# Kernel optimization log

Hardware: AMD Instinct MI355X
Metric: run time of the kernel (lower is better)

## Reference

```python
import jax, jax.numpy as jnp
import numpy as np
from jax import lax

KERNEL_SIZE = 3
SMOOTH_NR = 0.0
SMOOTH_DR = 1e-5


def _box_sum(x, k):
    # 3D box-filter sum with zero padding (matches F.conv3d padding=(k-1)//2),
    # x: [B, C, H, W, D]. 'SAME' padding with odd k and stride 1 == symmetric pad (k-1)//2.
    return lax.reduce_window(x, jnp.array(0.0, x.dtype), lax.add,
                             window_dimensions=(1, 1, k, k, k),
                             window_strides=(1, 1, 1, 1, 1),
                             padding='SAME')


def setup_inputs() -> dict:
    key = jax.random.key(0)
    k1, k2 = jax.random.split(key)
    shape = (2, 1, 192, 192, 192)
    pred = jax.random.uniform(k1, shape, dtype=jnp.float32)
    target = jax.random.uniform(k2, shape, dtype=jnp.float32)
    return {"pred": pred, "target": target}


def reference(pred, target):
    k = KERNEL_SIZE
    kvol = float(k ** 3)
    # Local means of I, J, I^2, J^2, I*J (box filter divided by kernel volume,
    # mirroring the torch code's avg_filt grouped conv over the 5C-channel interm).
    mI = _box_sum(pred, k) / kvol
    mJ = _box_sum(target, k) / kvol
    mII = _box_sum(pred * pred, k) / kvol
    mJJ = _box_sum(target * target, k) / kvol
    mIJ = _box_sum(pred * target, k) / kvol
    # Fused NCC reduction (cc3d_fwd_interm_v1): convert means back to
    # windowed sums-based cross/variance terms using kernel_vol.
    cross = kvol * (mIJ - mI * mJ)
    p_var = kvol * (mII - mI * mI)
    t_var = kvol * (mJJ - mJ * mJ)
    ncc = (cross * cross + SMOOTH_NR) / (t_var * p_var + SMOOTH_DR)
    # reduction='mean', loss is negated squared local ZNCC
    return -jnp.mean(ncc)
```

## Files before the change

kernel.cpp:

```cpp
#include <hip/hip_runtime.h>

#define DIMB 2
#define DIMS 192
#define DPT 4
#define TX 16
#define TY 16
#define HCHUNK 6
#define ROWF 72
#define ARR_F 432
#define SLAB_F 1024

#define GLOAD_LDS16(gp, lp) __builtin_amdgcn_global_load_lds( \
    (const __attribute__((address_space(1))) void*)(gp),      \
    (__attribute__((address_space(3))) void*)(lp), 16, 0, 0)

#define WAITV(n) asm volatile("s_waitcnt vmcnt(" #n ")" ::: "memory")
#define LGKM0    asm volatile("s_waitcnt lgkmcnt(0)" ::: "memory")

__device__ __forceinline__ float dpp_left(float x) {
    const int i = __float_as_int(x);
    return __int_as_float(__builtin_amdgcn_update_dpp(i, i, 0x111, 0xf, 0xf, false));
}
__device__ __forceinline__ float dpp_right(float x) {
    const int i = __float_as_int(x);
    return __int_as_float(__builtin_amdgcn_update_dpp(i, i, 0x101, 0xf, 0xf, false));
}

__device__ __forceinline__ float ncc_row3(const float (&Pm)[5][DPT],
                                          const float (&Pc)[5][DPT],
                                          const float (&Pn)[5][DPT])
{
    const float inv = 1.0f / 27.0f;
    float acc = 0.f;
#pragma unroll
    for (int j = 0; j < DPT; ++j) {
        const float sI  = Pm[0][j] + Pc[0][j] + Pn[0][j];
        const float sJ  = Pm[1][j] + Pc[1][j] + Pn[1][j];
        const float sII = Pm[2][j] + Pc[2][j] + Pn[2][j];
        const float sJJ = Pm[3][j] + Pc[3][j] + Pn[3][j];
        const float sIJ = Pm[4][j] + Pc[4][j] + Pn[4][j];
        const float uI = sI * inv;
        const float uJ = sJ * inv;
        const float cross = sIJ - uI * sJ;
        const float pvar  = sII - uI * sI;
        const float tvar  = sJJ - uJ * sJ;
        acc += (cross * cross) * __builtin_amdgcn_rcpf(tvar * pvar + 1e-5f);
    }
    return acc;
}

__global__ __launch_bounds__(256)
void FusedLocalNormalizedCrossCorrelationLoss_37838661877790_kernel(
    const float* __restrict__ pred, const float* __restrict__ targ,
    double* __restrict__ acc_out)
{
    __shared__ float L[4][3][SLAB_F];

    const int tx = threadIdx.x, ty = threadIdx.y;
    const int tid = ty * TX + tx;
    const int lane = tid & 63, wv = tid >> 6;
    const int tyw = ty & 3;
    const int d0b = blockIdx.x * (TX * DPT);
    const int w0  = blockIdx.y * TY;
    const int bz  = blockIdx.z;
    const int b   = bz >> 5;
    const int h0  = (bz & 31) * HCHUNK;

    int co[4]; const float* ab[4];
#pragma unroll
    for (int c = 0; c < 4; ++c) {
        const int fi = c * 256 + lane * 4;
        const int a  = (fi >= ARR_F) ? 1 : 0;
        int fi2 = fi - a * ARR_F;
        if (fi2 > ARR_F - 4) fi2 = ARR_F - 4;
        const int r = fi2 / ROWF, cl = fi2 % ROWF;
        int gd = d0b - 4 + cl;
        gd = gd < 0 ? 0 : (gd > DIMS - 4 ? DIMS - 4 : gd);
        int wr = w0 - 1 + 4 * wv + r;
        wr = wr < 0 ? 0 : (wr > DIMS - 1 ? DIMS - 1 : wr);
        co[c] = wr * DIMS + gd;
        ab[c] = a ? targ : pred;
    }

    auto stage = [&](int slot, int hh) {
        const int hhc = hh < 0 ? 0 : (hh > DIMS - 1 ? DIMS - 1 : hh);
        const size_t po = ((size_t)b * DIMS + hhc) * (DIMS * DIMS);
        float* lb = &L[wv][slot][0];
#pragma unroll
        for (int c = 0; c < 4; ++c)
            GLOAD_LDS16(ab[c] + po + co[c], lb + c * 256);
    };

    const bool lo_mask = (tx == 0)      && (blockIdx.x == 0);
    const bool hi_mask = (tx == TX - 1) && (blockIdx.x == gridDim.x - 1);
    const int rb0 = 4 * tx;

    auto plane = [&](int slot, int hh, float (&P)[5][DPT]) {
#pragma unroll
        for (int c5 = 0; c5 < 5; ++c5)
#pragma unroll
            for (int j = 0; j < DPT; ++j) P[c5][j] = 0.f;
        if (hh < 0 || hh >= DIMS) return;
        const float* Lp = &L[wv][slot][0];
        const float* Lt = Lp + ARR_F;
#pragma unroll
        for (int dw = 0; dw < 3; ++dw) {
            const int wr = w0 + ty + dw - 1;
            if (wr < 0 || wr >= DIMS) continue;
            const int rb = (tyw + dw) * ROWF + rb0;
            const float4 pm = *reinterpret_cast<const float4*>(Lp + rb + 4);
            const float4 tm = *reinterpret_cast<const float4*>(Lt + rb + 4);
            float p0 = dpp_left (pm.w);
            float p5 = dpp_right(pm.x);
            float t0 = dpp_left (tm.w);
            float t5 = dpp_right(tm.x);
            if (tx == 0)      { p0 = Lp[rb + 3]; t0 = Lt[rb + 3]; }
            if (tx == TX - 1) { p5 = Lp[rb + 8]; t5 = Lt[rb + 8]; }
            if (lo_mask) { p0 = 0.f; t0 = 0.f; }
            if (hi_mask) { p5 = 0.f; t5 = 0.f; }
            const float pv[6] = {p0, pm.x, pm.y, pm.z, pm.w, p5};
            const float tv[6] = {t0, tm.x, tm.y, tm.z, tm.w, t5};
            float pp[6], tt[6], pt[6];
#pragma unroll
            for (int k = 0; k < 6; ++k) {
                pp[k] = pv[k] * pv[k];
                tt[k] = tv[k] * tv[k];
                pt[k] = pv[k] * tv[k];
            }
#define WSUM(dst, a)                                            \
            { const float c12 = a[1] + a[2], c34 = a[3] + a[4]; \
              dst[0] += a[0] + c12; dst[1] += c12 + a[3];       \
              dst[2] += a[2] + c34; dst[3] += c34 + a[5]; }
            WSUM(P[0], pv)
            WSUM(P[1], tv)
            WSUM(P[2], pp)
            WSUM(P[3], tt)
            WSUM(P[4], pt)
#undef WSUM
        }
    };

    float PA[5][DPT], PB[5][DPT], PC[5][DPT];
    float acc = 0.f;

    stage(0, h0 - 1);
    stage(1, h0);
    stage(2, h0 + 1);
    WAITV(8); plane(0, h0 - 1, PA); LGKM0; stage(0, h0 + 2);
    WAITV(8); plane(1, h0,     PB); LGKM0; stage(1, h0 + 3);
    WAITV(8); plane(2, h0 + 1, PC); LGKM0; stage(2, h0 + 4);
    acc += ncc_row3(PA, PB, PC);
    WAITV(8); plane(0, h0 + 2, PA); LGKM0; stage(0, h0 + 5);
    acc += ncc_row3(PB, PC, PA);
    WAITV(8); plane(1, h0 + 3, PB); LGKM0; stage(1, h0 + 6);
    acc += ncc_row3(PC, PA, PB);
    WAITV(8); plane(2, h0 + 4, PC);
    acc += ncc_row3(PA, PB, PC);
    WAITV(4); plane(0, h0 + 5, PA);
    acc += ncc_row3(PB, PC, PA);
    WAITV(0); plane(1, h0 + 6, PB);
    acc += ncc_row3(PC, PA, PB);

#pragma unroll
    for (int off = 32; off > 0; off >>= 1)
        acc += __shfl_down(acc, off, 64);
    __shared__ float wacc[4];
    if ((tid & 63) == 0) wacc[tid >> 6] = acc;
    __syncthreads();
    if (tid == 0) {
        const double s = (double)wacc[0] + (double)wacc[1]
                       + (double)wacc[2] + (double)wacc[3];
        atomicAdd(acc_out, s);
    }
}

__global__ void ncc_finalize(const double* __restrict__ acc,
                             float* __restrict__ out)
{
    const double n = (double)((size_t)DIMB * DIMS * DIMS * DIMS);
    out[0] = (float)(-acc[0] / n);
}

extern "C" void kernel_launch(void* const* d_in, const int* in_sizes, int n_in,
                              void* d_out, int out_size, void* d_ws, size_t ws_size,
                              hipStream_t stream) {
    const float* pred = (const float*)d_in[0];
    const float* targ = (const float*)d_in[1];
    double* acc = (double*)d_ws;

    hipMemsetAsync(d_ws, 0, sizeof(double), stream);

    dim3 block(TX, TY, 1);
    dim3 grid(DIMS / (TX * DPT), DIMS / TY, DIMB * (DIMS / HCHUNK));
    FusedLocalNormalizedCrossCorrelationLoss_37838661877790_kernel
        <<<grid, block, 0, stream>>>(pred, targ, acc);
    ncc_finalize<<<1, 1, 0, stream>>>(acc, (float*)d_out);
}
```

Before: 156.5 us.

## Fold finalize into main kernel via last-block counter and zero-fill LDS halo rows

Removes the separate finalize kernel launch by having the last block, detected with an atomic counter, compute the final mean. It also replaces the per-row W-boundary branch in plane() by zeroing the out-of-range halo rows in LDS after staging, and initialises the accumulators on the first row instead of a separate zeroing pass. This drops one launch and some per-thread branching, in exchange for extra LDS stores in the edge blocks and a fence plus an atomic per block.

```diff
diff --git a/kernel.cpp b/kernel.cpp
--- a/kernel.cpp
+++ b/kernel.cpp
@@ -9,6 +9,7 @@
 #define ROWF 72
 #define ARR_F 432
 #define SLAB_F 1024
+#define NBLOCKS ((DIMS/(TX*DPT)) * (DIMS/TY) * (DIMB*(DIMS/HCHUNK)))
 
 #define GLOAD_LDS16(gp, lp) __builtin_amdgcn_global_load_lds( \
     (const __attribute__((address_space(1))) void*)(gp),      \
@@ -52,7 +53,8 @@
 __global__ __launch_bounds__(256)
 void FusedLocalNormalizedCrossCorrelationLoss_37838661877790_kernel(
     const float* __restrict__ pred, const float* __restrict__ targ,
-    double* __restrict__ acc_out)
+    double* __restrict__ acc_out, unsigned int* __restrict__ cnt,
+    float* __restrict__ out)
 {
     __shared__ float L[4][3][SLAB_F];
 
@@ -91,22 +93,39 @@
             GLOAD_LDS16(ab[c] + po + co[c], lb + c * 256);
     };
 
+    const bool zlo = (wv == 0) && (blockIdx.y == 0);
+    const bool zhi = (wv == 3) && (blockIdx.y == gridDim.y - 1);
+    int zoff = -1;
+    if (zlo) {
+        if (lane < 18)      zoff = lane * 4;
+        else if (lane < 36) zoff = ARR_F + (lane - 18) * 4;
+    } else if (zhi) {
+        if (lane < 18)      zoff = 5 * ROWF + lane * 4;
+        else if (lane < 36) zoff = ARR_F + 5 * ROWF + (lane - 18) * 4;
+    }
+    auto zfix = [&](int slot) {
+        if (zoff >= 0)
+            *reinterpret_cast<float4*>(&L[wv][slot][zoff]) =
+                make_float4(0.f, 0.f, 0.f, 0.f);
+    };
+
     const bool lo_mask = (tx == 0)      && (blockIdx.x == 0);
     const bool hi_mask = (tx == TX - 1) && (blockIdx.x == gridDim.x - 1);
     const int rb0 = 4 * tx;
 
     auto plane = [&](int slot, int hh, float (&P)[5][DPT]) {
-#pragma unroll
-        for (int c5 = 0; c5 < 5; ++c5)
-#pragma unroll
-            for (int j = 0; j < DPT; ++j) P[c5][j] = 0.f;
-        if (hh < 0 || hh >= DIMS) return;
+        if (hh < 0 || hh >= DIMS) {
+#pragma unroll
+            for (int c5 = 0; c5 < 5; ++c5)
+#pragma unroll
+                for (int j = 0; j < DPT; ++j) P[c5][j] = 0.f;
+            return;
+        }
         const float* Lp = &L[wv][slot][0];
         const float* Lt = Lp + ARR_F;
 #pragma unroll
         for (int dw = 0; dw < 3; ++dw) {
-            const int wr = w0 + ty + dw - 1;
-            if (wr < 0 || wr >= DIMS) continue;
+            const bool first = (dw == 0);
             const int rb = (tyw + dw) * ROWF + rb0;
             const float4 pm = *reinterpret_cast<const float4*>(Lp + rb + 4);
             const float4 tm = *reinterpret_cast<const float4*>(Lt + rb + 4);
@@ -127,10 +146,14 @@
                 tt[k] = tv[k] * tv[k];
                 pt[k] = pv[k] * tv[k];
             }
-#define WSUM(dst, a)                                            \
-            { const float c12 = a[1] + a[2], c34 = a[3] + a[4]; \
-              dst[0] += a[0] + c12; dst[1] += c12 + a[3];       \
-              dst[2] += a[2] + c34; dst[3] += c34 + a[5]; }
+#define WSUM(dst, a)                                                   \
+            { const float c12 = a[1] + a[2], c34 = a[3] + a[4];        \
+              const float s0 = a[0] + c12, s1 = c12 + a[3];            \
+              const float s2 = a[2] + c34, s3 = c34 + a[5];            \
+              if (first) { dst[0] = s0;  dst[1] = s1;                  \
+                           dst[2] = s2;  dst[3] = s3; }                \
+              else       { dst[0] += s0; dst[1] += s1;                 \
+                           dst[2] += s2; dst[3] += s3; } }
             WSUM(P[0], pv)
             WSUM(P[1], tv)
             WSUM(P[2], pp)
@@ -146,19 +169,19 @@
     stage(0, h0 - 1);
     stage(1, h0);
     stage(2, h0 + 1);
-    WAITV(8); plane(0, h0 - 1, PA); LGKM0; stage(0, h0 + 2);
-    WAITV(8); plane(1, h0,     PB); LGKM0; stage(1, h0 + 3);
-    WAITV(8); plane(2, h0 + 1, PC); LGKM0; stage(2, h0 + 4);
+    WAITV(8); zfix(0); plane(0, h0 - 1, PA); LGKM0; stage(0, h0 + 2);
+    WAITV(8); zfix(1); plane(1, h0,     PB); LGKM0; stage(1, h0 + 3);
+    WAITV(8); zfix(2); plane(2, h0 + 1, PC); LGKM0; stage(2, h0 + 4);
     acc += ncc_row3(PA, PB, PC);
-    WAITV(8); plane(0, h0 + 2, PA); LGKM0; stage(0, h0 + 5);
+    WAITV(8); zfix(0); plane(0, h0 + 2, PA); LGKM0; stage(0, h0 + 5);
     acc += ncc_row3(PB, PC, PA);
-    WAITV(8); plane(1, h0 + 3, PB); LGKM0; stage(1, h0 + 6);
+    WAITV(8); zfix(1); plane(1, h0 + 3, PB); LGKM0; stage(1, h0 + 6);
     acc += ncc_row3(PC, PA, PB);
-    WAITV(8); plane(2, h0 + 4, PC);
+    WAITV(8); zfix(2); plane(2, h0 + 4, PC);
     acc += ncc_row3(PA, PB, PC);
-    WAITV(4); plane(0, h0 + 5, PA);
+    WAITV(4); zfix(0); plane(0, h0 + 5, PA);
     acc += ncc_row3(PB, PC, PA);
-    WAITV(0); plane(1, h0 + 6, PB);
+    WAITV(0); zfix(1); plane(1, h0 + 6, PB);
     acc += ncc_row3(PC, PA, PB);
 
 #pragma unroll
@@ -171,14 +194,14 @@
         const double s = (double)wacc[0] + (double)wacc[1]
                        + (double)wacc[2] + (double)wacc[3];
         atomicAdd(acc_out, s);
-    }
-}
-
-__global__ void ncc_finalize(const double* __restrict__ acc,
-                             float* __restrict__ out)
-{
-    const double n = (double)((size_t)DIMB * DIMS * DIMS * DIMS);
-    out[0] = (float)(-acc[0] / n);
+        __threadfence();
+        const unsigned int done = atomicAdd(cnt, 1u);
+        if (done == (unsigned int)(NBLOCKS - 1)) {
+            const double tot = atomicAdd(acc_out, 0.0);
+            const double n = (double)((size_t)DIMB * DIMS * DIMS * DIMS);
+            out[0] = (float)(-tot / n);
+        }
+    }
 }
 
 extern "C" void kernel_launch(void* const* d_in, const int* in_sizes, int n_in,
@@ -187,12 +210,12 @@
     const float* pred = (const float*)d_in[0];
     const float* targ = (const float*)d_in[1];
     double* acc = (double*)d_ws;
-
-    hipMemsetAsync(d_ws, 0, sizeof(double), stream);
+    unsigned int* cnt = (unsigned int*)((char*)d_ws + sizeof(double));
+
+    hipMemsetAsync(d_ws, 0, sizeof(double) + sizeof(unsigned int) + 4, stream);
 
     dim3 block(TX, TY, 1);
     dim3 grid(DIMS / (TX * DPT), DIMS / TY, DIMB * (DIMS / HCHUNK));
     FusedLocalNormalizedCrossCorrelationLoss_37838661877790_kernel
-        <<<grid, block, 0, stream>>>(pred, targ, acc);
-    ncc_finalize<<<1, 1, 0, stream>>>(acc, (float*)d_out);
-}
+        <<<grid, block, 0, stream>>>(pred, targ, acc, cnt, (float*)d_out);
+}
```

After: 226.7 us. +44.9%, slower.
